# Kernel tuning notes

Hardware: AMD Instinct MI355X
Metric: run time of the kernel (lower is better)

Reference implementation:

```python
import jax, jax.numpy as jnp
import numpy as np

N, E, HID, H, L, R = 20000, 160000, 512, 8, 4, 128
DK = HID // H
SCALE = 1.0 / np.sqrt(DK)
EPS = 1e-5


def setup_inputs() -> dict:
    key = jax.random.key(0)
    ks = jax.random.split(key, 24)
    p = lambda i, shape: jax.random.normal(ks[i], shape, jnp.float32) * 0.02
    return {
        'x': jax.random.normal(ks[0], (N, HID), jnp.float32),
        'relations': jax.random.randint(ks[1], (E,), 0, R),
        'src': jax.random.randint(ks[2], (E,), 0, N),
        'dst': jax.random.randint(ks[3], (E,), 0, N),
        'rel_embed': p(4, (R, HID)),
        'Wq': p(5, (L, HID, HID)), 'bq': jnp.zeros((L, HID), jnp.float32),
        'Wk': p(6, (L, HID, HID)), 'bk': jnp.zeros((L, HID), jnp.float32),
        'Wv': p(7, (L, HID, HID)), 'bv': jnp.zeros((L, HID), jnp.float32),
        'Wo': p(8, (L, HID, HID)), 'bo': jnp.zeros((L, HID), jnp.float32),
        'W1': p(9, (L, HID, 4 * HID)), 'b1': jnp.zeros((L, 4 * HID), jnp.float32),
        'W2': p(10, (L, 4 * HID, HID)), 'b2': jnp.zeros((L, HID), jnp.float32),
        'ln1_g': jnp.ones((L, HID), jnp.float32), 'ln1_b': jnp.zeros((L, HID), jnp.float32),
        'ln2_g': jnp.ones((L, HID), jnp.float32), 'ln2_b': jnp.zeros((L, HID), jnp.float32),
    }


def _ln(x, g, b):
    m = x.mean(-1, keepdims=True)
    v = jnp.square(x - m).mean(-1, keepdims=True)
    return (x - m) * jax.lax.rsqrt(v + EPS) * g + b


def _layer(x, rh, src, dst, Wq, bq, Wk, bk, Wv, bv, Wo, bo, W1, b1, W2, b2, g1, bb1, g2, bb2):
    # rh: (E, H, DK) per-edge relation features
    q = (x @ Wq + bq).reshape(N, H, DK)
    k = (x @ Wk + bk).reshape(N, H, DK)
    v = (x @ Wv + bv).reshape(N, H, DK)
    # edge score: ((k_src + r) . q_dst) / sqrt(d_k)   -> (E, H)
    score = jnp.einsum('ehd,ehd->eh', k[src] + rh, q[dst]) * SCALE
    # segment softmax over incoming edges of each dst node
    smax = jax.ops.segment_max(score, dst, num_segments=N)
    smax = jnp.where(jnp.isfinite(smax), smax, 0.0)  # nodes with no in-edges
    ex = jnp.exp(score - smax[dst])                   # (E, H)
    z = jax.ops.segment_sum(ex, dst, num_segments=N)  # (N, H)
    wv = jax.ops.segment_sum(ex[:, :, None] * (v[src] + rh), dst, num_segments=N)  # (N, H, DK)
    o = wv / (z[:, :, None] + 1e-9)
    o = o.reshape(N, HID) @ Wo + bo
    h = _ln(x + o, g1, bb1)
    ff = jax.nn.relu(h @ W1 + b1) @ W2 + b2
    return _ln(h + ff, g2, bb2)


def reference(x, relations, src, dst, rel_embed, Wq, bq, Wk, bk, Wv, bv, Wo, bo, W1, b1, W2, b2, ln1_g, ln1_b, ln2_g, ln2_b):
    lg_x = rel_embed[relations]            # (E, HID), shared across layers
    rh = lg_x.reshape(E, H, DK)
    for i in range(L):
        x = _layer(x, rh, src, dst, Wq[i], bq[i], Wk[i], bk[i], Wv[i], bv[i],
                   Wo[i], bo[i], W1[i], b1[i], W2[i], b2[i],
                   ln1_g[i], ln1_b[i], ln2_g[i], ln2_b[i])
    return x
```

## Files before the change

kernel.cpp:

```cpp
#include <hip/hip_runtime.h>
#include <cstdint>
#include <cstddef>

#define N_NODES 20000
#define N_EDGES 160000
#define HIDDEN  512
#define NHEAD   8
#define HDK     64
#define NLAYER  4
#define FFDIM   2048
#define ATT_SCALE 0.125f
#define S1C 262144
#define S2C 1048576
#define WLYR (4 * S1C + 2 * S2C)

typedef float  f4  __attribute__((ext_vector_type(4)));
typedef short  s8v __attribute__((ext_vector_type(8)));
typedef __bf16 b8v __attribute__((ext_vector_type(8)));

template <typename V>
__device__ inline auto mfma_try(V a, V b, f4 c, int)
    -> decltype(__builtin_amdgcn_mfma_f32_16x16x32_bf16(a, b, c, 0, 0, 0)) {
  return __builtin_amdgcn_mfma_f32_16x16x32_bf16(a, b, c, 0, 0, 0);
}
template <typename V>
__device__ inline f4 mfma_try(V a, V b, f4 c, long) {
  return __builtin_amdgcn_mfma_f32_16x16x32_bf16(
      __builtin_bit_cast(b8v, a), __builtin_bit_cast(b8v, b), c, 0, 0, 0);
}
__device__ inline f4 mfma_bf16(s8v a, s8v b, f4 c) { return mfma_try(a, b, c, 0); }

__device__ __forceinline__ unsigned short f2bf(float f) {
  unsigned u = __builtin_bit_cast(unsigned, f);
  u += 0x7FFFu + ((u >> 16) & 1u);
  return (unsigned short)(u >> 16);
}
__device__ __forceinline__ float bf2f(unsigned short u) {
  return __builtin_bit_cast(float, (unsigned)u << 16);
}

#define GLOAD_LDS16(gp, lp)                                                   \
  __builtin_amdgcn_global_load_lds(                                           \
      (const __attribute__((address_space(1))) void*)(gp),                    \
      (__attribute__((address_space(3))) void*)(lp), 16, 0, 0)

__global__ void cast_kernel(const float* __restrict__ in, unsigned short* __restrict__ out, int n) {
  int i = blockIdx.x * blockDim.x + threadIdx.x;
  if (i < n) out[i] = f2bf(in[i]);
}

__global__ void weight_prep_kernel(const float* __restrict__ Wq, const float* __restrict__ Wk,
                                   const float* __restrict__ Wv, const float* __restrict__ Wo_,
                                   const float* __restrict__ W1, const float* __restrict__ W2,
                                   const float* __restrict__ bq, const float* __restrict__ bk,
                                   const float* __restrict__ bv,
                                   unsigned short* __restrict__ wAll, float* __restrict__ bqkvAll) {
  int l = blockIdx.x / 3078;
  int id = blockIdx.x % 3078;
  unsigned short* wqkv = wAll + (size_t)l * WLYR;
  unsigned short* wo = wqkv + 3 * S1C;
  unsigned short* w1 = wo + S1C;
  unsigned short* w2 = w1 + S2C;
  if (id >= 3072) {
    int i = (id - 3072) * 256 + threadIdx.y * 32 + threadIdx.x;
    float* bqkv = bqkvAll + l * 1536;
    if (i < 512) bqkv[i] = bq[l * 512 + i];
    else if (i < 1024) bqkv[i] = bk[l * 512 + i - 512];
    else if (i < 1536) bqkv[i] = bv[l * 512 + i - 1024];
    return;
  }
  const float* in; unsigned short* out; int K, N, bx, by;
  if (id < 1024) {
    int m = id >> 8, t = id & 255;
    in = ((m == 0) ? Wq : (m == 1) ? Wk : (m == 2) ? Wv : Wo_) + (size_t)l * S1C;
    out = (m == 3) ? wo : wqkv + m * S1C;
    K = 512; N = 512; bx = t & 15; by = t >> 4;
  } else if (id < 2048) {
    int t = id - 1024;
    in = W1 + (size_t)l * S2C; out = w1; K = 512; N = 2048; bx = t & 63; by = t >> 6;
  } else {
    int t = id - 2048;
    in = W2 + (size_t)l * S2C; out = w2; K = 2048; N = 512; bx = t & 15; by = t >> 4;
  }
  __shared__ float t32[32][33];
  int tx = threadIdx.x, ty = threadIdx.y;
  int n0 = bx * 32, k0 = by * 32;
#pragma unroll
  for (int i = 0; i < 32; i += 8)
    t32[ty + i][tx] = in[(size_t)(k0 + ty + i) * N + n0 + tx];
  __syncthreads();
#pragma unroll
  for (int i = 0; i < 32; i += 8)
    out[(size_t)(n0 + ty + i) * K + k0 + tx] = f2bf(t32[tx][ty + i]);
}

#define BM 128
#define BN 128
#define BK 64

template <bool OBF16>
__global__ __launch_bounds__(256, 3) void gemm_bf16(
    const unsigned short* __restrict__ A, const unsigned short* __restrict__ Bt,
    const float* __restrict__ bias, void* __restrict__ Cp,
    int M, int K, int N, int relu) {
  __shared__ __align__(16) unsigned short smem[16384];
  unsigned short* As = smem;
  unsigned short* Bs = smem + 8192;
  int tid = threadIdx.x;
  int wave = tid >> 6, lane = tid & 63;
  int quad = lane >> 4, l16 = lane & 15;
  int wm = (wave >> 1) * 64, wn = (wave & 1) * 64;

  int T = gridDim.x * gridDim.y;
  int i = blockIdx.y * gridDim.x + blockIdx.x;
  int C = T >> 3;
  int w = (i < (C << 3)) ? ((i & 7) * C + (i >> 3)) : i;
  int bx = w % gridDim.x, by = w / gridDim.x;
  int m0 = by * BM, n0 = bx * BN;

  f4 acc[4][4];
#pragma unroll
  for (int i2 = 0; i2 < 4; ++i2)
#pragma unroll
    for (int j = 0; j < 4; ++j) acc[i2][j] = (f4){0.f, 0.f, 0.f, 0.f};

  int rbase = wave * 8 + (lane >> 3);
  int q8 = (lane & 7) ^ ((lane >> 3) & 7);
  const unsigned short* aptr[4];
  const unsigned short* bptr[4];
#pragma unroll
  for (int j = 0; j < 4; ++j) {
    int r = j * 32 + rbase;
    int gm = m0 + r; if (gm >= M) gm = M - 1;
    aptr[j] = A + (size_t)gm * K + q8 * 8;
    bptr[j] = Bt + (size_t)(n0 + r) * K + q8 * 8;
  }

  int nk = K >> 6;
  for (int ks = 0; ks < nk; ++ks) {
#pragma unroll
    for (int j = 0; j < 4; ++j)
      GLOAD_LDS16(aptr[j], &As[j * 2048 + wave * 512]);
#pragma unroll
    for (int j = 0; j < 4; ++j)
      GLOAD_LDS16(bptr[j], &Bs[j * 2048 + wave * 512]);
#pragma unroll
    for (int j = 0; j < 4; ++j) { aptr[j] += BK; bptr[j] += BK; }
    __syncthreads();
#pragma unroll
    for (int s = 0; s < 2; ++s) {
      s8v af[4], bfr[4];
#pragma unroll
      for (int i2 = 0; i2 < 4; ++i2) {
        int ra = wm + i2 * 16 + l16;
        int rb = wn + i2 * 16 + l16;
        af[i2]  = *(const s8v*)(&As[ra * 64 + ((((s << 2) | quad) ^ (ra & 7)) * 8)]);
        bfr[i2] = *(const s8v*)(&Bs[rb * 64 + ((((s << 2) | quad) ^ (rb & 7)) * 8)]);
      }
#pragma unroll
      for (int mi = 0; mi < 4; ++mi)
#pragma unroll
        for (int ni = 0; ni < 4; ++ni)
          acc[mi][ni] = mfma_bf16(af[mi], bfr[ni], acc[mi][ni]);
    }
    __syncthreads();
  }

  if constexpr (OBF16) {
    unsigned short* Cs = smem + wave * 1088;
    float bvv[4];
#pragma unroll
    for (int ni = 0; ni < 4; ++ni) bvv[ni] = bias[n0 + wn + ni * 16 + l16];
    int row_l = lane >> 2, cg = lane & 3;
#pragma unroll
    for (int mi = 0; mi < 4; ++mi) {
#pragma unroll
      for (int ni = 0; ni < 4; ++ni) {
#pragma unroll
        for (int r = 0; r < 4; ++r) {
          float val = acc[mi][ni][r] + bvv[ni];
          if (relu) val = fmaxf(val, 0.f);
          Cs[(quad * 4 + r) * 68 + ni * 16 + l16] = f2bf(val);
        }
      }
      s8v v0 = *(const s8v*)(&Cs[row_l * 68 + cg * 16]);
      s8v v1 = *(const s8v*)(&Cs[row_l * 68 + cg * 16 + 8]);
      int grow = m0 + wm + mi * 16 + row_l;
      if (grow < M) {
        unsigned short* cp = (unsigned short*)Cp + (size_t)grow * N + n0 + wn + cg * 16;
        *(s8v*)cp = v0;
        *(s8v*)(cp + 8) = v1;
      }
    }
  } else {
#pragma unroll
    for (int ni = 0; ni < 4; ++ni) {
      int col = n0 + wn + ni * 16 + l16;
      float bv = bias[col];
#pragma unroll
      for (int mi = 0; mi < 4; ++mi) {
#pragma unroll
        for (int r = 0; r < 4; ++r) {
          int row = m0 + wm + mi * 16 + quad * 4 + r;
          if (row < M) {
            float val = acc[mi][ni][r] + bv;
            if (relu) val = fmaxf(val, 0.f);
            ((float*)Cp)[(size_t)row * N + col] = val;
          }
        }
      }
    }
  }
}

__global__ void hist_kernel(const int* __restrict__ dst, int* __restrict__ cnt, int E) {
  int e = blockIdx.x * blockDim.x + threadIdx.x;
  if (e < E) atomicAdd(&cnt[dst[e]], 1);
}

__global__ void scan_kernel(const int* __restrict__ cnt, int* __restrict__ offs, int n) {
  __shared__ int sh[1024];
  __shared__ int carry_sh;
  int tid = threadIdx.x;
  if (tid == 0) carry_sh = 0;
  __syncthreads();
  for (int base = 0; base < n; base += 1024) {
    int v = (base + tid < n) ? cnt[base + tid] : 0;
    sh[tid] = v;
    __syncthreads();
    for (int s = 1; s < 1024; s <<= 1) {
      int t = (tid >= s) ? sh[tid - s] : 0;
      __syncthreads();
      sh[tid] += t;
      __syncthreads();
    }
    int carry = carry_sh;
    if (base + tid < n) offs[base + tid] = carry + sh[tid] - v;
    __syncthreads();
    if (tid == 1023) carry_sh = carry + sh[1023];
    __syncthreads();
  }
  if (tid == 0) offs[n] = carry_sh;
}

__global__ void scatter_kernel(const int* __restrict__ dst, const int* __restrict__ src,
                               const int* __restrict__ relations, const int* __restrict__ offs,
                               int* __restrict__ cursor, int* __restrict__ esrc,
                               int* __restrict__ erel, int E) {
  int e = blockIdx.x * blockDim.x + threadIdx.x;
  if (e < E) {
    int d = dst[e];
    int pos = offs[d] + atomicAdd(&cursor[d], 1);
    esrc[pos] = src[e];
    erel[pos] = relations[e];
  }
}

__global__ void edge_attn_kernel(const unsigned short* __restrict__ q,
                                 const unsigned short* __restrict__ k,
                                 const unsigned short* __restrict__ v,
                                 const unsigned short* __restrict__ relb,
                                 const int* __restrict__ offs,
                                 const int* __restrict__ esrc,
                                 const int* __restrict__ erel,
                                 unsigned short* __restrict__ o, int Nn, int STR) {
  int wid = (blockIdx.x * blockDim.x + threadIdx.x) >> 6;
  int lane = threadIdx.x & 63;
  if (wid >= Nn) return;
  int base = (lane >> 3) * HDK + (lane & 7) * 8;

  s8v qv = *(const s8v*)(q + (size_t)wid * STR + base);
  float qf[8];
#pragma unroll
  for (int j = 0; j < 8; ++j) qf[j] = bf2f((unsigned short)qv[j]);

  int beg = offs[wid], end = offs[wid + 1];
  float m = -1e30f, z = 0.f;
  float acc[8];
#pragma unroll
  for (int j = 0; j < 8; ++j) acc[j] = 0.f;

  s8v kv = {}, vv = {}, rv = {};
  if (beg < end) {
    int s0 = esrc[beg], r0 = erel[beg];
    kv = *(const s8v*)(k + (size_t)s0 * STR + base);
    vv = *(const s8v*)(v + (size_t)s0 * STR + base);
    rv = *(const s8v*)(relb + (size_t)r0 * HIDDEN + base);
  }
  for (int i = beg; i < end; ++i) {
    s8v kc = kv, vc = vv, rc = rv;
    if (i + 1 < end) {
      int sn = esrc[i + 1], rn = erel[i + 1];
      kv = *(const s8v*)(k + (size_t)sn * STR + base);
      vv = *(const s8v*)(v + (size_t)sn * STR + base);
      rv = *(const s8v*)(relb + (size_t)rn * HIDDEN + base);
    }
    float rf[8], p = 0.f;
#pragma unroll
    for (int j = 0; j < 8; ++j) {
      rf[j] = bf2f((unsigned short)rc[j]);
      p += (bf2f((unsigned short)kc[j]) + rf[j]) * qf[j];
    }
    p += __shfl_xor(p, 1, 64);
    p += __shfl_xor(p, 2, 64);
    p += __shfl_xor(p, 4, 64);
    p *= ATT_SCALE;
    float mn = fmaxf(m, p);
    float a = __expf(m - mn);
    float wgt = __expf(p - mn);
    z = z * a + wgt;
#pragma unroll
    for (int j = 0; j < 8; ++j)
      acc[j] = acc[j] * a + wgt * (bf2f((unsigned short)vc[j]) + rf[j]);
    m = mn;
  }
  float rz = 1.f / (z + 1e-9f);
  s8v ov;
#pragma unroll
  for (int j = 0; j < 8; ++j) ov[j] = (short)f2bf(acc[j] * rz);
  *(s8v*)(o + (size_t)wid * HIDDEN + base) = ov;
}

template <bool WF32>
__global__ void ln_kernel(const unsigned short* __restrict__ xp, const unsigned short* __restrict__ y,
                          const float* __restrict__ g, const float* __restrict__ b,
                          float* __restrict__ outf, unsigned short* __restrict__ outb, int Nn) {
  int wid = (blockIdx.x * blockDim.x + threadIdx.x) >> 6;
  int lane = threadIdx.x & 63;
  if (wid >= Nn) return;
  float vals[8];
  float sum = 0.f;
#pragma unroll
  for (int j = 0; j < 8; ++j) {
    int idx = j * 64 + lane;
    vals[j] = bf2f(xp[(size_t)wid * HIDDEN + idx]) + bf2f(y[(size_t)wid * HIDDEN + idx]);
    sum += vals[j];
  }
#pragma unroll
  for (int off = 32; off; off >>= 1) sum += __shfl_xor(sum, off, 64);
  float mean = sum * (1.f / 512.f);
  float sq = 0.f;
#pragma unroll
  for (int j = 0; j < 8; ++j) { float d = vals[j] - mean; sq += d * d; }
#pragma unroll
  for (int off = 32; off; off >>= 1) sq += __shfl_xor(sq, off, 64);
  float rstd = rsqrtf(sq * (1.f / 512.f) + 1e-5f);
#pragma unroll
  for (int j = 0; j < 8; ++j) {
    int idx = j * 64 + lane;
    float val = (vals[j] - mean) * rstd * g[idx] + b[idx];
    if constexpr (WF32) outf[(size_t)wid * HIDDEN + idx] = val;
    outb[(size_t)wid * HIDDEN + idx] = f2bf(val);
  }
}

extern "C" void kernel_launch(void* const* d_in, const int* in_sizes, int n_in,
                              void* d_out, int out_size, void* d_ws, size_t ws_size,
                              hipStream_t stream) {
  const float* x0        = (const float*)d_in[0];
  const int*   relations = (const int*)d_in[1];
  const int*   src       = (const int*)d_in[2];
  const int*   dst       = (const int*)d_in[3];
  const float* rel_embed = (const float*)d_in[4];
  const float* Wq = (const float*)d_in[5];  const float* bq = (const float*)d_in[6];
  const float* Wk = (const float*)d_in[7];  const float* bk = (const float*)d_in[8];
  const float* Wv = (const float*)d_in[9];  const float* bv = (const float*)d_in[10];
  const float* Wo = (const float*)d_in[11]; const float* bo = (const float*)d_in[12];
  const float* W1 = (const float*)d_in[13]; const float* b1 = (const float*)d_in[14];
  const float* W2 = (const float*)d_in[15]; const float* b2 = (const float*)d_in[16];
  const float* g1  = (const float*)d_in[17]; const float* bb1 = (const float*)d_in[18];
  const float* g2  = (const float*)d_in[19]; const float* bb2 = (const float*)d_in[20];
  float* xout = (float*)d_out;

  const size_t S1 = S1C;
  const size_t S2 = S2C;
  const size_t NH = (size_t)N_NODES * HIDDEN;

  unsigned short* wAll = (unsigned short*)d_ws;
  float* bqkvAll = (float*)(wAll + (size_t)NLAYER * WLYR);
  unsigned short* arena = (unsigned short*)(bqkvAll + NLAYER * 1536);
  unsigned short* qkvb = arena;
  unsigned short* ob   = arena + 3 * NH;
  unsigned short* ff1  = arena;
  unsigned short* proj = arena;
  unsigned short* hbb = arena + 4 * NH;
  unsigned short* xb  = hbb + NH;
  unsigned short* projb = xb + NH;
  unsigned short* relb  = projb + NH;
  int* cnt    = (int*)(relb + 65536);
  int* offs   = cnt + N_NODES;
  int* cursor = offs + N_NODES + 1;
  int* esrc   = cursor + N_NODES;
  int* erel   = esrc + N_EDGES;

  hipMemsetAsync(cnt, 0, N_NODES * sizeof(int), stream);
  hipMemsetAsync(cursor, 0, N_NODES * sizeof(int), stream);
  hist_kernel<<<(N_EDGES + 255) / 256, 256, 0, stream>>>(dst, cnt, N_EDGES);
  scan_kernel<<<1, 1024, 0, stream>>>(cnt, offs, N_NODES);
  scatter_kernel<<<(N_EDGES + 255) / 256, 256, 0, stream>>>(dst, src, relations, offs, cursor, esrc, erel, N_EDGES);
  cast_kernel<<<(int)((NH + 255) / 256), 256, 0, stream>>>(x0, xb, (int)NH);
  cast_kernel<<<256, 256, 0, stream>>>(rel_embed, relb, 65536);
  dim3 tb(32, 8);
  weight_prep_kernel<<<NLAYER * 3078, tb, 0, stream>>>(Wq, Wk, Wv, Wo, W1, W2, bq, bk, bv,
                                                       wAll, bqkvAll);

  const int MBc = (N_NODES + BM - 1) / BM;

  for (int l = 0; l < NLAYER; ++l) {
    unsigned short* wqkv = wAll + (size_t)l * WLYR;
    unsigned short* wo = wqkv + 3 * S1;
    unsigned short* w1 = wo + S1;
    unsigned short* w2 = w1 + S2;
    float* bqkv = bqkvAll + l * 1536;
    gemm_bf16<true><<<dim3(12, MBc), 256, 0, stream>>>(xb, wqkv, bqkv, qkvb, N_NODES, 512, 1536, 0);
    edge_attn_kernel<<<(N_NODES + 3) / 4, 256, 0, stream>>>(qkvb, qkvb + 512, qkvb + 1024,
                                                            relb, offs, esrc, erel, ob, N_NODES, 1536);
    gemm_bf16<true><<<dim3(4, MBc), 256, 0, stream>>>(ob, wo, bo + l * 512, proj, N_NODES, 512, 512, 0);
    ln_kernel<false><<<N_NODES / 4, 256, 0, stream>>>(xb, proj, g1 + l * 512, bb1 + l * 512, nullptr, hbb, N_NODES);
    gemm_bf16<true><<<dim3(16, MBc), 256, 0, stream>>>(hbb, w1, b1 + l * 2048, ff1, N_NODES, 512, 2048, 1);
    gemm_bf16<true><<<dim3(4, MBc), 256, 0, stream>>>(ff1, w2, b2 + l * 512, projb, N_NODES, 2048, 512, 0);
    if (l == NLAYER - 1)
      ln_kernel<true><<<N_NODES / 4, 256, 0, stream>>>(hbb, projb, g2 + l * 512, bb2 + l * 512, xout, xb, N_NODES);
    else
      ln_kernel<false><<<N_NODES / 4, 256, 0, stream>>>(hbb, projb, g2 + l * 512, bb2 + l * 512, nullptr, xb, N_NODES);
  }
}
```

Baseline: 1.219 ms.

## Pre-tile weights into MFMA fragment layout and load B directly to registers

The weight conversion kernel now writes bf16 weights in a 16x8-blocked layout matching the MFMA B-fragment, so each lane can load its B operand with one contiguous 16-byte global load. The GEMM drops the B tile from LDS, halving shared memory use and LDS traffic, and loads B fragments straight into registers each K-step. In exchange each wave reloads its B fragments from global/L2 with no sharing across the two M-waves, and the global-load latency is exposed without explicit prefetching.

```diff
diff --git a/kernel.cpp b/kernel.cpp
--- a/kernel.cpp
+++ b/kernel.cpp
@@ -85,13 +85,17 @@
   __shared__ float t32[32][33];
   int tx = threadIdx.x, ty = threadIdx.y;
   int n0 = bx * 32, k0 = by * 32;
+  int Kc = K >> 3;
 #pragma unroll
   for (int i = 0; i < 32; i += 8)
     t32[ty + i][tx] = in[(size_t)(k0 + ty + i) * N + n0 + tx];
   __syncthreads();
 #pragma unroll
-  for (int i = 0; i < 32; i += 8)
-    out[(size_t)(n0 + ty + i) * K + k0 + tx] = f2bf(t32[tx][ty + i]);
+  for (int i = 0; i < 32; i += 8) {
+    int n = n0 + ty + i, k = k0 + tx;
+    size_t idx = ((size_t)(n >> 4) * Kc + (k >> 3)) * 128 + (n & 15) * 8 + (k & 7);
+    out[idx] = f2bf(t32[tx][ty + i]);
+  }
 }
 
 #define BM 128
@@ -103,9 +107,7 @@
     const unsigned short* __restrict__ A, const unsigned short* __restrict__ Bt,
     const float* __restrict__ bias, void* __restrict__ Cp,
     int M, int K, int N, int relu) {
-  __shared__ __align__(16) unsigned short smem[16384];
-  unsigned short* As = smem;
-  unsigned short* Bs = smem + 8192;
+  __shared__ __align__(16) unsigned short As[8192];
   int tid = threadIdx.x;
   int wave = tid >> 6, lane = tid & 63;
   int quad = lane >> 4, l16 = lane & 15;
@@ -127,47 +129,53 @@
   int rbase = wave * 8 + (lane >> 3);
   int q8 = (lane & 7) ^ ((lane >> 3) & 7);
   const unsigned short* aptr[4];
-  const unsigned short* bptr[4];
 #pragma unroll
   for (int j = 0; j < 4; ++j) {
     int r = j * 32 + rbase;
     int gm = m0 + r; if (gm >= M) gm = M - 1;
     aptr[j] = A + (size_t)gm * K + q8 * 8;
-    bptr[j] = Bt + (size_t)(n0 + r) * K + q8 * 8;
-  }
+  }
+
+  int Kc = K >> 3;
+  const unsigned short* bbase = Bt + quad * 128 + l16 * 8;
+  size_t nioff[4];
+#pragma unroll
+  for (int i2 = 0; i2 < 4; ++i2)
+    nioff[i2] = ((size_t)((n0 >> 4) + (wn >> 4) + i2) * Kc) * 128;
 
   int nk = K >> 6;
   for (int ks = 0; ks < nk; ++ks) {
 #pragma unroll
     for (int j = 0; j < 4; ++j)
       GLOAD_LDS16(aptr[j], &As[j * 2048 + wave * 512]);
-#pragma unroll
-    for (int j = 0; j < 4; ++j)
-      GLOAD_LDS16(bptr[j], &Bs[j * 2048 + wave * 512]);
-#pragma unroll
-    for (int j = 0; j < 4; ++j) { aptr[j] += BK; bptr[j] += BK; }
+    s8v bfr[2][4];
+#pragma unroll
+    for (int s = 0; s < 2; ++s)
+#pragma unroll
+      for (int i2 = 0; i2 < 4; ++i2)
+        bfr[s][i2] = *(const s8v*)(bbase + nioff[i2] + (size_t)ks * 1024 + s * 512);
+#pragma unroll
+    for (int j = 0; j < 4; ++j) aptr[j] += BK;
     __syncthreads();
 #pragma unroll
     for (int s = 0; s < 2; ++s) {
-      s8v af[4], bfr[4];
+      s8v af[4];
 #pragma unroll
       for (int i2 = 0; i2 < 4; ++i2) {
         int ra = wm + i2 * 16 + l16;
-        int rb = wn + i2 * 16 + l16;
-        af[i2]  = *(const s8v*)(&As[ra * 64 + ((((s << 2) | quad) ^ (ra & 7)) * 8)]);
-        bfr[i2] = *(const s8v*)(&Bs[rb * 64 + ((((s << 2) | quad) ^ (rb & 7)) * 8)]);
+        af[i2] = *(const s8v*)(&As[ra * 64 + ((((s << 2) | quad) ^ (ra & 7)) * 8)]);
       }
 #pragma unroll
       for (int mi = 0; mi < 4; ++mi)
 #pragma unroll
         for (int ni = 0; ni < 4; ++ni)
-          acc[mi][ni] = mfma_bf16(af[mi], bfr[ni], acc[mi][ni]);
+          acc[mi][ni] = mfma_bf16(af[mi], bfr[s][ni], acc[mi][ni]);
     }
     __syncthreads();
   }
 
   if constexpr (OBF16) {
-    unsigned short* Cs = smem + wave * 1088;
+    unsigned short* Cs = As + wave * 1088;
     float bvv[4];
 #pragma unroll
     for (int ni = 0; ni < 4; ++ni) bvv[ni] = bias[n0 + wn + ni * 16 + l16];
```

New measurement: 1.215 ms. No clear change (-0.3%).
